# Optimization experiments

Hardware: AMD Instinct MI355X
Metric: run time of the kernel (lower is better)

The kernel has to match this reference:

```python
import jax, jax.numpy as jnp
import numpy as np

N = 262144      # active voxels
K = 27          # 3^3 kernel offsets
C_IN = 64
C_OUT = 64
EPS = 1e-5      # BatchNorm eps (torch default)


def setup_inputs() -> dict:
    key = jax.random.key(0)
    k1, k2, k3, k4, k5 = jax.random.split(key, 5)
    features = jax.random.normal(k1, (N, C_IN), dtype=jnp.float32)
    # kernel map: for each offset k and output point i, index of the input
    # neighbor; value == N means 'no neighbor' (maps to a zero pad row)
    nbr_idx = jax.random.randint(k2, (K, N), 0, N + 1)
    weight = jax.random.normal(k3, (K, C_IN, C_OUT), dtype=jnp.float32) * (1.0 / np.sqrt(K * C_IN))
    gamma = jax.random.uniform(k4, (C_OUT,), dtype=jnp.float32, minval=0.5, maxval=1.5)
    beta = jax.random.normal(k5, (C_OUT,), dtype=jnp.float32) * 0.1
    return {"features": features, "nbr_idx": nbr_idx, "weight": weight,
            "gamma": gamma, "beta": beta}


def reference(features, nbr_idx, weight, gamma, beta):
    # zero pad row so idx == N contributes nothing (missing neighbor)
    padded = jnp.concatenate(
        [features, jnp.zeros((1, features.shape[1]), features.dtype)], axis=0)

    def body(acc, kw):
        idx, w = kw                      # idx: [N], w: [C_in, C_out]
        gathered = padded[idx]           # [N, C_in] irregular gather
        return acc + gathered @ w, None  # GEMM + scatter-accumulate

    acc0 = jnp.zeros((features.shape[0], weight.shape[2]), features.dtype)
    out, _ = jax.lax.scan(body, acc0, (nbr_idx, weight))  # [N, C_out]

    # BatchNorm1d over points (training-mode batch statistics)
    mean = jnp.mean(out, axis=0)
    var = jnp.var(out, axis=0)
    out = (out - mean) * jax.lax.rsqrt(var + EPS) * gamma + beta
    # ReLU
    return jnp.maximum(out, 0.0)
```

## Files before the change

kernel.cpp:

```cpp
#include <hip/hip_runtime.h>
#include <hip/hip_bf16.h>
#include <stdint.h>

#define N_PTS 262144
#define KOFF 27
#define CIN 64
#define COUT 64
#define EPS 1e-5f

typedef __attribute__((ext_vector_type(8))) short short8;
typedef __attribute__((ext_vector_type(4))) float f32x4;
typedef __attribute__((ext_vector_type(4))) unsigned short ushort4v;

static __device__ __forceinline__ unsigned short f32_to_bf16(float f) {
    union { float f; unsigned int u; } v; v.f = f;
    unsigned int u = v.u;
    unsigned int rounded = u + 0x7FFF + ((u >> 16) & 1);
    return (unsigned short)(rounded >> 16);
}

__global__ void k_packW(const float* __restrict__ w, unsigned short* __restrict__ pw) {
    int tid = blockIdx.x * blockDim.x + threadIdx.x;
    if (tid >= KOFF * 4096) return;
    int e = tid & 7;
    int l = (tid >> 3) & 63;
    int t = (tid >> 9) & 3;
    int s = (tid >> 11) & 1;
    int k = tid >> 12;
    int cin  = s * 32 + (l >> 4) * 8 + e;
    int cout = t * 16 + (l & 15);
    pw[tid] = f32_to_bf16(w[(k * CIN + cin) * COUT + cout]);
}

__global__ void k_feat2bf16(const float* __restrict__ feat, unsigned short* __restrict__ out) {
    int gid = blockIdx.x * blockDim.x + threadIdx.x;
    const int total4 = (N_PTS + 1) * CIN / 4;
    if (gid >= total4) return;
    int base = gid * 4;
    ushort4v o;
    if (base < N_PTS * CIN) {
        f32x4 f = *reinterpret_cast<const f32x4*>(feat + base);
        o[0] = f32_to_bf16(f[0]); o[1] = f32_to_bf16(f[1]);
        o[2] = f32_to_bf16(f[2]); o[3] = f32_to_bf16(f[3]);
    } else {
        o[0] = 0; o[1] = 0; o[2] = 0; o[3] = 0;
    }
    *reinterpret_cast<ushort4v*>(out + base) = o;
}

__global__ __launch_bounds__(256) void k_conv(
    const unsigned short* __restrict__ feat,
    const int* __restrict__ nbr,
    const unsigned short* __restrict__ pw,
    float* __restrict__ conv_out,
    float* __restrict__ partials)
{
    __shared__ unsigned short ldsB[4096];
    __shared__ float s_sum[64], s_sq[64];

    const int tid = threadIdx.x;
    const int l  = tid & 63;
    const int w  = tid >> 6;
    const int lr = l & 15;
    const int lg = l >> 4;
    const int rowbase = blockIdx.x * 128 + w * 32;
    const int r0 = rowbase + lr;
    const int r1 = r0 + 16;
    const int lane_cin = lg * 8;

    if (tid < 64) { s_sum[tid] = 0.f; s_sq[tid] = 0.f; }

    f32x4 acc[2][4] = {};

    const short8* pwv = reinterpret_cast<const short8*>(pw);
    short8* ldsv = reinterpret_cast<short8*>(ldsB);

    for (int k = 0; k < KOFF; ++k) {
        __syncthreads();
        short8 w0 = pwv[k * 512 + tid];
        short8 w1 = pwv[k * 512 + 256 + tid];
        ldsv[tid] = w0;
        ldsv[256 + tid] = w1;

        int i0 = nbr[k * N_PTS + r0];
        int i1 = nbr[k * N_PTS + r1];
        const short8* fr0 = reinterpret_cast<const short8*>(feat + i0 * 64 + lane_cin);
        const short8* fr1 = reinterpret_cast<const short8*>(feat + i1 * 64 + lane_cin);
        short8 a00 = fr0[0];
        short8 a01 = fr0[4];
        short8 a10 = fr1[0];
        short8 a11 = fr1[4];

        __syncthreads();
        #pragma unroll
        for (int s = 0; s < 2; ++s) {
            short8 a0 = s ? a01 : a00;
            short8 a1 = s ? a11 : a10;
            #pragma unroll
            for (int t = 0; t < 4; ++t) {
                short8 b = ldsv[(s * 4 + t) * 64 + l];
                acc[0][t] = __builtin_amdgcn_mfma_f32_16x16x32_bf16(a0, b, acc[0][t], 0, 0, 0);
                acc[1][t] = __builtin_amdgcn_mfma_f32_16x16x32_bf16(a1, b, acc[1][t], 0, 0, 0);
            }
        }
    }

    const int orow_base = rowbase + lg * 4;
    #pragma unroll
    for (int t = 0; t < 4; ++t) {
        const int c = t * 16 + lr;
        float psum = 0.f, psq = 0.f;
        #pragma unroll
        for (int m = 0; m < 2; ++m) {
            #pragma unroll
            for (int e = 0; e < 4; ++e) {
                float v = acc[m][t][e];
                conv_out[(orow_base + m * 16 + e) * 64 + c] = v;
                psum += v; psq += v * v;
            }
        }
        atomicAdd(&s_sum[c], psum);
        atomicAdd(&s_sq[c], psq);
    }
    __syncthreads();
    if (tid < 64) {
        partials[blockIdx.x * 128 + tid]      = s_sum[tid];
        partials[blockIdx.x * 128 + 64 + tid] = s_sq[tid];
    }
}

__global__ void k_stats(const float* __restrict__ partials,
                        const float* __restrict__ gamma,
                        const float* __restrict__ beta,
                        float* __restrict__ ss, int nblocks) {
    __shared__ float s_red[2];
    const int c = blockIdx.x;
    const int tid = threadIdx.x;
    if (tid < 2) s_red[tid] = 0.f;
    __syncthreads();
    float sum = 0.f, sq = 0.f;
    for (int b = tid; b < nblocks; b += blockDim.x) {
        sum += partials[b * 128 + c];
        sq  += partials[b * 128 + 64 + c];
    }
    #pragma unroll
    for (int off = 32; off > 0; off >>= 1) {
        sum += __shfl_down(sum, off, 64);
        sq  += __shfl_down(sq,  off, 64);
    }
    if ((tid & 63) == 0) { atomicAdd(&s_red[0], sum); atomicAdd(&s_red[1], sq); }
    __syncthreads();
    if (tid == 0) {
        float mean  = s_red[0] / (float)N_PTS;
        float var   = s_red[1] / (float)N_PTS - mean * mean;
        float scale = gamma[c] * rsqrtf(var + EPS);
        ss[c]      = scale;
        ss[64 + c] = beta[c] - mean * scale;
    }
}

__global__ void k_bnrelu(float* __restrict__ out, const float* __restrict__ ss) {
    int gid = blockIdx.x * blockDim.x + threadIdx.x;
    int base = gid * 4;
    int c0 = base & 63;
    f32x4 v  = *reinterpret_cast<f32x4*>(out + base);
    f32x4 sc = *reinterpret_cast<const f32x4*>(ss + c0);
    f32x4 sh = *reinterpret_cast<const f32x4*>(ss + 64 + c0);
    f32x4 r;
    #pragma unroll
    for (int j = 0; j < 4; ++j) r[j] = fmaxf(v[j] * sc[j] + sh[j], 0.f);
    *reinterpret_cast<f32x4*>(out + base) = r;
}

extern "C" void kernel_launch(void* const* d_in, const int* in_sizes, int n_in,
                              void* d_out, int out_size, void* d_ws, size_t ws_size,
                              hipStream_t stream) {
    const float* features = (const float*)d_in[0];
    const int*   nbr      = (const int*)d_in[1];
    const float* weight   = (const float*)d_in[2];
    const float* gamma    = (const float*)d_in[3];
    const float* beta     = (const float*)d_in[4];
    float* out = (float*)d_out;
    char* ws = (char*)d_ws;

    const size_t off_feat = 0;
    const size_t off_pw   = 33554560;
    const size_t off_part = off_pw + 221184;
    const size_t off_ss   = off_part + 1048576;
    unsigned short* feat16   = (unsigned short*)(ws + off_feat);
    unsigned short* pw       = (unsigned short*)(ws + off_pw);
    float*          partials = (float*)(ws + off_part);
    float*          ss       = (float*)(ws + off_ss);

    const int nblocks = N_PTS / 128;

    k_packW<<<(KOFF * 4096 + 255) / 256, 256, 0, stream>>>(weight, pw);
    k_feat2bf16<<<((N_PTS + 1) * CIN / 4 + 255) / 256, 256, 0, stream>>>(features, feat16);
    k_conv<<<nblocks, 256, 0, stream>>>(feat16, nbr, pw, out, partials);
    k_stats<<<64, 256, 0, stream>>>(partials, gamma, beta, ss, nblocks);
    k_bnrelu<<<N_PTS * COUT / 4 / 256, 256, 0, stream>>>(out, ss);
}
```

Measured before the change: 194.4 us.

## Double-buffer weights via direct global-to-LDS loads and prefetch next gather

The conv kernel now double-buffers the per-offset weight tile in LDS, filling it with global_load_lds so the data skips registers. It also prefetches the next offset's neighbor indices and gathered feature rows while the current MFMAs run. This removes one of the two barriers per offset and is meant to hide the gather latency behind compute. In exchange it uses more registers for the prefetched operands, which may lower occupancy.

```diff
diff --git a/kernel.cpp b/kernel.cpp
--- a/kernel.cpp
+++ b/kernel.cpp
@@ -11,6 +11,11 @@
 typedef __attribute__((ext_vector_type(8))) short short8;
 typedef __attribute__((ext_vector_type(4))) float f32x4;
 typedef __attribute__((ext_vector_type(4))) unsigned short ushort4v;
+
+typedef __attribute__((address_space(3))) unsigned int lds_u32;
+typedef __attribute__((address_space(1))) const unsigned int glb_u32;
+
+#define GLDS16(g, s) __builtin_amdgcn_global_load_lds((glb_u32*)(g), (lds_u32*)(s), 16, 0, 0)
 
 static __device__ __forceinline__ unsigned short f32_to_bf16(float f) {
     union { float f; unsigned int u; } v; v.f = f;
@@ -55,7 +60,7 @@
     float* __restrict__ conv_out,
     float* __restrict__ partials)
 {
-    __shared__ unsigned short ldsB[4096];
+    __shared__ short8 ldsv[2][512];
     __shared__ float s_sum[64], s_sq[64];
 
     const int tid = threadIdx.x;
@@ -71,37 +76,50 @@
     if (tid < 64) { s_sum[tid] = 0.f; s_sq[tid] = 0.f; }
 
     f32x4 acc[2][4] = {};
-
     const short8* pwv = reinterpret_cast<const short8*>(pw);
-    short8* ldsv = reinterpret_cast<short8*>(ldsB);
-
-    for (int k = 0; k < KOFF; ++k) {
+
+    int i0  = nbr[r0];
+    int i1  = nbr[r1];
+    int i0n = nbr[N_PTS + r0];
+    int i1n = nbr[N_PTS + r1];
+
+    GLDS16(pwv + w * 64 + l,       &ldsv[0][w * 64]);
+    GLDS16(pwv + 256 + w * 64 + l, &ldsv[0][256 + w * 64]);
+
+    {
+        const short8* f0 = reinterpret_cast<const short8*>(feat + i0 * 64 + lane_cin);
+        const short8* f1 = reinterpret_cast<const short8*>(feat + i1 * 64 + lane_cin);
+        short8 a00 = f0[0], a01 = f0[4], a10 = f1[0], a11 = f1[4];
         __syncthreads();
-        short8 w0 = pwv[k * 512 + tid];
-        short8 w1 = pwv[k * 512 + 256 + tid];
-        ldsv[tid] = w0;
-        ldsv[256 + tid] = w1;
-
-        int i0 = nbr[k * N_PTS + r0];
-        int i1 = nbr[k * N_PTS + r1];
-        const short8* fr0 = reinterpret_cast<const short8*>(feat + i0 * 64 + lane_cin);
-        const short8* fr1 = reinterpret_cast<const short8*>(feat + i1 * 64 + lane_cin);
-        short8 a00 = fr0[0];
-        short8 a01 = fr0[4];
-        short8 a10 = fr1[0];
-        short8 a11 = fr1[4];
-
-        __syncthreads();
-        #pragma unroll
-        for (int s = 0; s < 2; ++s) {
-            short8 a0 = s ? a01 : a00;
-            short8 a1 = s ? a11 : a10;
+
+        for (int k = 0; k < KOFF; ++k) {
+            const int cur = k & 1;
+            short8 b00 = {}, b01 = {}, b10 = {}, b11 = {};
+            if (k + 1 < KOFF) {
+                GLDS16(pwv + (k + 1) * 512 + w * 64 + l,       &ldsv[cur ^ 1][w * 64]);
+                GLDS16(pwv + (k + 1) * 512 + 256 + w * 64 + l, &ldsv[cur ^ 1][256 + w * 64]);
+                const short8* g0 = reinterpret_cast<const short8*>(feat + i0n * 64 + lane_cin);
+                const short8* g1 = reinterpret_cast<const short8*>(feat + i1n * 64 + lane_cin);
+                b00 = g0[0]; b01 = g0[4]; b10 = g1[0]; b11 = g1[4];
+                if (k + 2 < KOFF) {
+                    i0n = nbr[(k + 2) * N_PTS + r0];
+                    i1n = nbr[(k + 2) * N_PTS + r1];
+                }
+            }
+            const short8* cb = &ldsv[cur][l];
             #pragma unroll
-            for (int t = 0; t < 4; ++t) {
-                short8 b = ldsv[(s * 4 + t) * 64 + l];
-                acc[0][t] = __builtin_amdgcn_mfma_f32_16x16x32_bf16(a0, b, acc[0][t], 0, 0, 0);
-                acc[1][t] = __builtin_amdgcn_mfma_f32_16x16x32_bf16(a1, b, acc[1][t], 0, 0, 0);
+            for (int s = 0; s < 2; ++s) {
+                short8 a0 = s ? a01 : a00;
+                short8 a1 = s ? a11 : a10;
+                #pragma unroll
+                for (int t = 0; t < 4; ++t) {
+                    short8 b = cb[(s * 4 + t) * 64];
+                    acc[0][t] = __builtin_amdgcn_mfma_f32_16x16x32_bf16(a0, b, acc[0][t], 0, 0, 0);
+                    acc[1][t] = __builtin_amdgcn_mfma_f32_16x16x32_bf16(a1, b, acc[1][t], 0, 0, 0);
+                }
             }
+            __syncthreads();
+            a00 = b00; a01 = b01; a10 = b10; a11 = b11;
         }
     }
 
```

Result: slower. 198.6 us (+2.2%).

## Software-pipeline conv gather with triple-buffered async weight loads to LDS

Applied to the files above, without the earlier changes.

Restructures the conv main loop into a multi-stage software pipeline. Neighbor indices are prefetched several offsets ahead and feature rows are gathered two offsets ahead into registers. Weight tiles stream directly into a triple-buffered LDS region through global_load_lds, so each iteration needs one barrier with a hand-tuned vmcnt wait instead of two syncthreads around a blocking gather. The aim is to hide the irregular gather latency behind MFMA work. In exchange it uses more registers and LDS, and correctness depends on the hardcoded waitcnt count and the volatile index loads.

```diff
diff --git a/kernel.cpp b/kernel.cpp
--- a/kernel.cpp
+++ b/kernel.cpp
@@ -11,6 +11,10 @@
 typedef __attribute__((ext_vector_type(8))) short short8;
 typedef __attribute__((ext_vector_type(4))) float f32x4;
 typedef __attribute__((ext_vector_type(4))) unsigned short ushort4v;
+
+typedef __attribute__((address_space(3))) unsigned int lds_u32;
+typedef __attribute__((address_space(1))) const unsigned int glb_u32;
+#define GLDS16(g, s) __builtin_amdgcn_global_load_lds((glb_u32*)(g), (lds_u32*)(s), 16, 0, 0)
 
 static __device__ __forceinline__ unsigned short f32_to_bf16(float f) {
     union { float f; unsigned int u; } v; v.f = f;
@@ -55,7 +59,7 @@
     float* __restrict__ conv_out,
     float* __restrict__ partials)
 {
-    __shared__ unsigned short ldsB[4096];
+    __shared__ short ldsB[3][4096];
     __shared__ float s_sum[64], s_sq[64];
 
     const int tid = threadIdx.x;
@@ -71,38 +75,74 @@
     if (tid < 64) { s_sum[tid] = 0.f; s_sq[tid] = 0.f; }
 
     f32x4 acc[2][4] = {};
-
     const short8* pwv = reinterpret_cast<const short8*>(pw);
-    short8* ldsv = reinterpret_cast<short8*>(ldsB);
-
-    for (int k = 0; k < KOFF; ++k) {
-        __syncthreads();
-        short8 w0 = pwv[k * 512 + tid];
-        short8 w1 = pwv[k * 512 + 256 + tid];
-        ldsv[tid] = w0;
-        ldsv[256 + tid] = w1;
-
-        int i0 = nbr[k * N_PTS + r0];
-        int i1 = nbr[k * N_PTS + r1];
-        const short8* fr0 = reinterpret_cast<const short8*>(feat + i0 * 64 + lane_cin);
-        const short8* fr1 = reinterpret_cast<const short8*>(feat + i1 * 64 + lane_cin);
-        short8 a00 = fr0[0];
-        short8 a01 = fr0[4];
-        short8 a10 = fr1[0];
-        short8 a11 = fr1[4];
-
-        __syncthreads();
-        #pragma unroll
-        for (int s = 0; s < 2; ++s) {
-            short8 a0 = s ? a01 : a00;
-            short8 a1 = s ? a11 : a10;
-            #pragma unroll
-            for (int t = 0; t < 4; ++t) {
-                short8 b = ldsv[(s * 4 + t) * 64 + l];
-                acc[0][t] = __builtin_amdgcn_mfma_f32_16x16x32_bf16(a0, b, acc[0][t], 0, 0, 0);
-                acc[1][t] = __builtin_amdgcn_mfma_f32_16x16x32_bf16(a1, b, acc[1][t], 0, 0, 0);
-            }
-        }
+    const volatile int* vnbr = nbr;
+
+    int ia0 = vnbr[r0],          ia1 = vnbr[r1];
+    int ib0 = vnbr[N_PTS + r0],  ib1 = vnbr[N_PTS + r1];
+    short8 ac0 = {}, ac1 = {}, ac2 = {}, ac3 = {};
+    short8 an0 = {}, an1 = {}, an2 = {}, an3 = {};
+
+    #pragma unroll
+    for (int kk = 0; kk < KOFF + 2; ++kk) {
+        const int k = kk - 2;
+
+        {
+            int kg = k + 1; if (kg < 0) kg = 0; if (kg >= KOFF) kg = KOFF - 1;
+            const short8* src = pwv + kg * 512 + w * 128;
+            short* dst = &ldsB[(kk + 2) % 3][w * 1024];
+            GLDS16(src + l,      dst);
+            GLDS16(src + 64 + l, dst + 512);
+        }
+        short8 t0, t1, t2, t3;
+        {
+            const short8* g0 = reinterpret_cast<const short8*>(feat + ia0 * 64 + lane_cin);
+            const short8* g1 = reinterpret_cast<const short8*>(feat + ia1 * 64 + lane_cin);
+            t0 = g0[0]; t1 = g0[4]; t2 = g1[0]; t3 = g1[4];
+        }
+        int ic0, ic1;
+        {
+            const int ki = (k + 4) % KOFF;
+            ic0 = vnbr[ki * N_PTS + r0];
+            ic1 = vnbr[ki * N_PTS + r1];
+        }
+        __builtin_amdgcn_sched_barrier(0);
+
+        if (k >= 0) {
+            asm volatile("s_waitcnt vmcnt(14)" ::: "memory");
+            __builtin_amdgcn_s_barrier();
+            __builtin_amdgcn_sched_barrier(0);
+
+            const short8* cb = reinterpret_cast<const short8*>(&ldsB[(kk + 1) % 3][0]);
+            short8 b0 = cb[l];
+            short8 b1 = cb[64 + l];
+            short8 b2 = cb[128 + l];
+            short8 b3 = cb[192 + l];
+            short8 b4 = cb[256 + l];
+            short8 b5 = cb[320 + l];
+            short8 b6 = cb[384 + l];
+            short8 b7 = cb[448 + l];
+            acc[0][0] = __builtin_amdgcn_mfma_f32_16x16x32_bf16(ac0, b0, acc[0][0], 0, 0, 0);
+            acc[1][0] = __builtin_amdgcn_mfma_f32_16x16x32_bf16(ac2, b0, acc[1][0], 0, 0, 0);
+            acc[0][1] = __builtin_amdgcn_mfma_f32_16x16x32_bf16(ac0, b1, acc[0][1], 0, 0, 0);
+            acc[1][1] = __builtin_amdgcn_mfma_f32_16x16x32_bf16(ac2, b1, acc[1][1], 0, 0, 0);
+            acc[0][2] = __builtin_amdgcn_mfma_f32_16x16x32_bf16(ac0, b2, acc[0][2], 0, 0, 0);
+            acc[1][2] = __builtin_amdgcn_mfma_f32_16x16x32_bf16(ac2, b2, acc[1][2], 0, 0, 0);
+            acc[0][3] = __builtin_amdgcn_mfma_f32_16x16x32_bf16(ac0, b3, acc[0][3], 0, 0, 0);
+            acc[1][3] = __builtin_amdgcn_mfma_f32_16x16x32_bf16(ac2, b3, acc[1][3], 0, 0, 0);
+            acc[0][0] = __builtin_amdgcn_mfma_f32_16x16x32_bf16(ac1, b4, acc[0][0], 0, 0, 0);
+            acc[1][0] = __builtin_amdgcn_mfma_f32_16x16x32_bf16(ac3, b4, acc[1][0], 0, 0, 0);
+            acc[0][1] = __builtin_amdgcn_mfma_f32_16x16x32_bf16(ac1, b5, acc[0][1], 0, 0, 0);
+            acc[1][1] = __builtin_amdgcn_mfma_f32_16x16x32_bf16(ac3, b5, acc[1][1], 0, 0, 0);
+            acc[0][2] = __builtin_amdgcn_mfma_f32_16x16x32_bf16(ac1, b6, acc[0][2], 0, 0, 0);
+            acc[1][2] = __builtin_amdgcn_mfma_f32_16x16x32_bf16(ac3, b6, acc[1][2], 0, 0, 0);
+            acc[0][3] = __builtin_amdgcn_mfma_f32_16x16x32_bf16(ac1, b7, acc[0][3], 0, 0, 0);
+            acc[1][3] = __builtin_amdgcn_mfma_f32_16x16x32_bf16(ac3, b7, acc[1][3], 0, 0, 0);
+        }
+
+        ia0 = ib0; ia1 = ib1; ib0 = ic0; ib1 = ic1;
+        ac0 = an0; ac1 = an1; ac2 = an2; ac3 = an3;
+        an0 = t0;  an1 = t1;  an2 = t2;  an3 = t3;
     }
 
     const int orow_base = rowbase + lg * 4;
```

Result: slower. 198.8 us (+2.3%).

## Software-pipeline conv gather and weight loads in registers, drop LDS and block syncs

Applied to the files above, without the earlier changes.

The conv kernel now uses 128-thread blocks. Each wave loads its weight fragments straight from global memory into registers instead of staging them through LDS with two barriers per offset. The loop is software-pipelined: neighbor indices are prefetched two offsets ahead, and feature gathers and weights one offset ahead of the MFMAs, with sched_barriers separating the stages. BatchNorm statistics are reduced with wave shuffles and atomically added into 64 global group slots, so the stats kernel becomes a single small block. The trade-offs are higher register pressure, redundant per-wave weight loads from L2, and an extra memset.

```diff
diff --git a/kernel.cpp b/kernel.cpp
--- a/kernel.cpp
+++ b/kernel.cpp
@@ -48,114 +48,133 @@
     *reinterpret_cast<ushort4v*>(out + base) = o;
 }
 
-__global__ __launch_bounds__(256) void k_conv(
+__global__ __launch_bounds__(128, 3) void k_conv(
     const unsigned short* __restrict__ feat,
     const int* __restrict__ nbr,
     const unsigned short* __restrict__ pw,
     float* __restrict__ conv_out,
-    float* __restrict__ partials)
+    float* __restrict__ grp)
 {
-    __shared__ unsigned short ldsB[4096];
-    __shared__ float s_sum[64], s_sq[64];
-
     const int tid = threadIdx.x;
     const int l  = tid & 63;
     const int w  = tid >> 6;
     const int lr = l & 15;
     const int lg = l >> 4;
-    const int rowbase = blockIdx.x * 128 + w * 32;
+    const int wid = blockIdx.x * 2 + w;
+    const int rowbase = wid * 32;
     const int r0 = rowbase + lr;
     const int r1 = r0 + 16;
     const int lane_cin = lg * 8;
 
-    if (tid < 64) { s_sum[tid] = 0.f; s_sq[tid] = 0.f; }
-
     f32x4 acc[2][4] = {};
-
     const short8* pwv = reinterpret_cast<const short8*>(pw);
-    short8* ldsv = reinterpret_cast<short8*>(ldsB);
-
-    for (int k = 0; k < KOFF; ++k) {
-        __syncthreads();
-        short8 w0 = pwv[k * 512 + tid];
-        short8 w1 = pwv[k * 512 + 256 + tid];
-        ldsv[tid] = w0;
-        ldsv[256 + tid] = w1;
-
-        int i0 = nbr[k * N_PTS + r0];
-        int i1 = nbr[k * N_PTS + r1];
-        const short8* fr0 = reinterpret_cast<const short8*>(feat + i0 * 64 + lane_cin);
-        const short8* fr1 = reinterpret_cast<const short8*>(feat + i1 * 64 + lane_cin);
-        short8 a00 = fr0[0];
-        short8 a01 = fr0[4];
-        short8 a10 = fr1[0];
-        short8 a11 = fr1[4];
-
-        __syncthreads();
-        #pragma unroll
-        for (int s = 0; s < 2; ++s) {
-            short8 a0 = s ? a01 : a00;
-            short8 a1 = s ? a11 : a10;
-            #pragma unroll
-            for (int t = 0; t < 4; ++t) {
-                short8 b = ldsv[(s * 4 + t) * 64 + l];
-                acc[0][t] = __builtin_amdgcn_mfma_f32_16x16x32_bf16(a0, b, acc[0][t], 0, 0, 0);
-                acc[1][t] = __builtin_amdgcn_mfma_f32_16x16x32_bf16(a1, b, acc[1][t], 0, 0, 0);
-            }
-        }
+
+    int ia0 = nbr[r0],          ia1 = nbr[r1];
+    int ib0 = nbr[N_PTS + r0],  ib1 = nbr[N_PTS + r1];
+
+    short8 ac0 = {}, ac1 = {}, ac2 = {}, ac3 = {};
+    short8 an0 = {}, an1 = {}, an2 = {}, an3 = {};
+    short8 bc0 = {}, bc1 = {}, bc2 = {}, bc3 = {}, bc4 = {}, bc5 = {}, bc6 = {}, bc7 = {};
+    short8 bn0 = {}, bn1 = {}, bn2 = {}, bn3 = {}, bn4 = {}, bn5 = {}, bn6 = {}, bn7 = {};
+
+    #pragma unroll
+    for (int kk = 0; kk < KOFF + 2; ++kk) {
+        if (kk >= 1 && kk - 1 < KOFF) {
+            const short8* bb = pwv + (kk - 1) * 512 + l;
+            bn0 = bb[0];   bn1 = bb[64];  bn2 = bb[128]; bn3 = bb[192];
+            bn4 = bb[256]; bn5 = bb[320]; bn6 = bb[384]; bn7 = bb[448];
+        }
+        short8 t0 = {}, t1 = {}, t2 = {}, t3 = {};
+        if (kk < KOFF) {
+            const short8* g0 = reinterpret_cast<const short8*>(feat + ia0 * 64 + lane_cin);
+            const short8* g1 = reinterpret_cast<const short8*>(feat + ia1 * 64 + lane_cin);
+            t0 = g0[0]; t1 = g0[4]; t2 = g1[0]; t3 = g1[4];
+        }
+        int ic0 = 0, ic1 = 0;
+        if (kk + 2 < KOFF) {
+            ic0 = nbr[(kk + 2) * N_PTS + r0];
+            ic1 = nbr[(kk + 2) * N_PTS + r1];
+        }
+        __builtin_amdgcn_sched_barrier(0);
+
+        if (kk >= 2) {
+            acc[0][0] = __builtin_amdgcn_mfma_f32_16x16x32_bf16(ac0, bc0, acc[0][0], 0, 0, 0);
+            acc[1][0] = __builtin_amdgcn_mfma_f32_16x16x32_bf16(ac2, bc0, acc[1][0], 0, 0, 0);
+            acc[0][1] = __builtin_amdgcn_mfma_f32_16x16x32_bf16(ac0, bc1, acc[0][1], 0, 0, 0);
+            acc[1][1] = __builtin_amdgcn_mfma_f32_16x16x32_bf16(ac2, bc1, acc[1][1], 0, 0, 0);
+            acc[0][2] = __builtin_amdgcn_mfma_f32_16x16x32_bf16(ac0, bc2, acc[0][2], 0, 0, 0);
+            acc[1][2] = __builtin_amdgcn_mfma_f32_16x16x32_bf16(ac2, bc2, acc[1][2], 0, 0, 0);
+            acc[0][3] = __builtin_amdgcn_mfma_f32_16x16x32_bf16(ac0, bc3, acc[0][3], 0, 0, 0);
+            acc[1][3] = __builtin_amdgcn_mfma_f32_16x16x32_bf16(ac2, bc3, acc[1][3], 0, 0, 0);
+            acc[0][0] = __builtin_amdgcn_mfma_f32_16x16x32_bf16(ac1, bc4, acc[0][0], 0, 0, 0);
+            acc[1][0] = __builtin_amdgcn_mfma_f32_16x16x32_bf16(ac3, bc4, acc[1][0], 0, 0, 0);
+            acc[0][1] = __builtin_amdgcn_mfma_f32_16x16x32_bf16(ac1, bc5, acc[0][1], 0, 0, 0);
+            acc[1][1] = __builtin_amdgcn_mfma_f32_16x16x32_bf16(ac3, bc5, acc[1][1], 0, 0, 0);
+            acc[0][2] = __builtin_amdgcn_mfma_f32_16x16x32_bf16(ac1, bc6, acc[0][2], 0, 0, 0);
+            acc[1][2] = __builtin_amdgcn_mfma_f32_16x16x32_bf16(ac3, bc6, acc[1][2], 0, 0, 0);
+            acc[0][3] = __builtin_amdgcn_mfma_f32_16x16x32_bf16(ac1, bc7, acc[0][3], 0, 0, 0);
+            acc[1][3] = __builtin_amdgcn_mfma_f32_16x16x32_bf16(ac3, bc7, acc[1][3], 0, 0, 0);
+        }
+        __builtin_amdgcn_sched_barrier(0);
+
+        ia0 = ib0; ia1 = ib1; ib0 = ic0; ib1 = ic1;
+        ac0 = an0; ac1 = an1; ac2 = an2; ac3 = an3;
+        an0 = t0;  an1 = t1;  an2 = t2;  an3 = t3;
+        bc0 = bn0; bc1 = bn1; bc2 = bn2; bc3 = bn3;
+        bc4 = bn4; bc5 = bn5; bc6 = bn6; bc7 = bn7;
     }
 
     const int orow_base = rowbase + lg * 4;
+    float psum[4], psq[4];
     #pragma unroll
     for (int t = 0; t < 4; ++t) {
         const int c = t * 16 + lr;
-        float psum = 0.f, psq = 0.f;
+        float s = 0.f, q = 0.f;
         #pragma unroll
         for (int m = 0; m < 2; ++m) {
             #pragma unroll
             for (int e = 0; e < 4; ++e) {
                 float v = acc[m][t][e];
                 conv_out[(orow_base + m * 16 + e) * 64 + c] = v;
-                psum += v; psq += v * v;
+                s += v; q += v * v;
             }
         }
-        atomicAdd(&s_sum[c], psum);
-        atomicAdd(&s_sq[c], psq);
-    }
-    __syncthreads();
-    if (tid < 64) {
-        partials[blockIdx.x * 128 + tid]      = s_sum[tid];
-        partials[blockIdx.x * 128 + 64 + tid] = s_sq[tid];
-    }
-}
-
-__global__ void k_stats(const float* __restrict__ partials,
+        psum[t] = s; psq[t] = q;
+    }
+    #pragma unroll
+    for (int t = 0; t < 4; ++t) {
+        psum[t] += __shfl_xor(psum[t], 16, 64);
+        psum[t] += __shfl_xor(psum[t], 32, 64);
+        psq[t]  += __shfl_xor(psq[t],  16, 64);
+        psq[t]  += __shfl_xor(psq[t],  32, 64);
+    }
+    if (lg == 0) {
+        float* g = grp + (blockIdx.x & 63) * 128;
+        #pragma unroll
+        for (int t = 0; t < 4; ++t) {
+            const int c = t * 16 + lr;
+            atomicAdd(&g[c],      psum[t]);
+            atomicAdd(&g[64 + c], psq[t]);
+        }
+    }
+}
+
+__global__ void k_stats(const float* __restrict__ grp,
                         const float* __restrict__ gamma,
                         const float* __restrict__ beta,
-                        float* __restrict__ ss, int nblocks) {
-    __shared__ float s_red[2];
-    const int c = blockIdx.x;
-    const int tid = threadIdx.x;
-    if (tid < 2) s_red[tid] = 0.f;
+                        float* __restrict__ ss) {
+    __shared__ float red[128];
+    const int j = threadIdx.x;
+    float s = 0.f;
+    for (int g = 0; g < 64; ++g) s += grp[g * 128 + j];
+    red[j] = s;
     __syncthreads();
-    float sum = 0.f, sq = 0.f;
-    for (int b = tid; b < nblocks; b += blockDim.x) {
-        sum += partials[b * 128 + c];
-        sq  += partials[b * 128 + 64 + c];
-    }
-    #pragma unroll
-    for (int off = 32; off > 0; off >>= 1) {
-        sum += __shfl_down(sum, off, 64);
-        sq  += __shfl_down(sq,  off, 64);
-    }
-    if ((tid & 63) == 0) { atomicAdd(&s_red[0], sum); atomicAdd(&s_red[1], sq); }
-    __syncthreads();
-    if (tid == 0) {
-        float mean  = s_red[0] / (float)N_PTS;
-        float var   = s_red[1] / (float)N_PTS - mean * mean;
-        float scale = gamma[c] * rsqrtf(var + EPS);
-        ss[c]      = scale;
-        ss[64 + c] = beta[c] - mean * scale;
+    if (j < 64) {
+        float mean  = red[j] / (float)N_PTS;
+        float var   = red[64 + j] / (float)N_PTS - mean * mean;
+        float scale = gamma[j] * rsqrtf(var + EPS);
+        ss[j]      = scale;
+        ss[64 + j] = beta[j] - mean * scale;
     }
 }
 
@@ -185,18 +204,17 @@
 
     const size_t off_feat = 0;
     const size_t off_pw   = 33554560;
-    const size_t off_part = off_pw + 221184;
-    const size_t off_ss   = off_part + 1048576;
-    unsigned short* feat16   = (unsigned short*)(ws + off_feat);
-    unsigned short* pw       = (unsigned short*)(ws + off_pw);
-    float*          partials = (float*)(ws + off_part);
-    float*          ss       = (float*)(ws + off_ss);
-
-    const int nblocks = N_PTS / 128;
-
+    const size_t off_grp  = off_pw + 221184;
+    const size_t off_ss   = off_grp + 32768;
+    unsigned short* feat16 = (unsigned short*)(ws + off_feat);
+    unsigned short* pw     = (unsigned short*)(ws + off_pw);
+    float*          grp    = (float*)(ws + off_grp);
+    float*          ss     = (float*)(ws + off_ss);
+
+    hipMemsetAsync(grp, 0, 64 * 128 * sizeof(float), stream);
     k_packW<<<(KOFF * 4096 + 255) / 256, 256, 0, stream>>>(weight, pw);
     k_feat2bf16<<<((N_PTS + 1) * CIN / 4 + 255) / 256, 256, 0, stream>>>(features, feat16);
-    k_conv<<<nblocks, 256, 0, stream>>>(feat16, nbr, pw, out, partials);
-    k_stats<<<64, 256, 0, stream>>>(partials, gamma, beta, ss, nblocks);
+    k_conv<<<N_PTS / 64, 128, 0, stream>>>(feat16, nbr, pw, out, grp);
+    k_stats<<<1, 128, 0, stream>>>(grp, gamma, beta, ss);
     k_bnrelu<<<N_PTS * COUT / 4 / 256, 256, 0, stream>>>(out, ss);
 }
```

Measured after the change: 211.5 us. 1.09x slower.
